# Performance work log

Measured on AMD Instinct MI355X. Metric: run time of the kernel, lower is better.

The kernel has to match this reference:

```python
import jax, jax.numpy as jnp
import numpy as np

N_NODES = 50000
N_EDGES = 800000
D = 128
N_GRAPHS = 64
N_CLASSES = 10


def setup_inputs() -> dict:
    key = jax.random.key(0)
    ks = jax.random.split(key, 10)
    x = jax.random.normal(ks[0], (N_NODES, D), dtype=jnp.float32)
    edge_index = jax.random.randint(ks[1], (2, N_EDGES), 0, N_NODES, dtype=jnp.int64)
    batch = jnp.sort(jax.random.randint(ks[2], (N_NODES,), 0, N_GRAPHS, dtype=jnp.int64))
    s = 1.0 / np.sqrt(D)
    W1a = jax.random.uniform(ks[3], (D, D), jnp.float32, -s, s)
    W1b = jax.random.uniform(ks[4], (D, D), jnp.float32, -s, s)
    W2a = jax.random.uniform(ks[5], (D, D), jnp.float32, -s, s)
    W2b = jax.random.uniform(ks[6], (D, D), jnp.float32, -s, s)
    Wfc = jax.random.uniform(ks[7], (D, N_CLASSES), jnp.float32, -s, s)
    return {
        "x": x, "edge_index": edge_index, "batch": batch,
        "W1a": W1a, "b1a": jnp.zeros((D,), jnp.float32),
        "W1b": W1b, "b1b": jnp.zeros((D,), jnp.float32),
        "W2a": W2a, "b2a": jnp.zeros((D,), jnp.float32),
        "W2b": W2b, "b2b": jnp.zeros((D,), jnp.float32),
        "Wfc": Wfc, "bfc": jnp.zeros((N_CLASSES,), jnp.float32),
    }


def _gin_conv(x, src, dst, Wa, ba, Wb, bb):
    # sum aggregation of neighbor messages x[src] into dst (eps = 0)
    agg = jax.ops.segment_sum(x[src], dst, num_segments=N_NODES)
    h = x + agg  # (1 + eps) * x + sum_{j->i} x_j
    h = jax.nn.relu(h @ Wa + ba)
    h = jax.nn.relu(h @ Wb + bb)
    return h


def reference(x, edge_index, batch, W1a, b1a, W1b, b1b, W2a, b2a, W2b, b2b, Wfc, bfc):
    src, dst = edge_index[0], edge_index[1]
    h = _gin_conv(x, src, dst, W1a, b1a, W1b, b1b)
    h = _gin_conv(h, src, dst, W2a, b2a, W2b, b2b)
    # global mean pool over graphs
    sums = jax.ops.segment_sum(h, batch, num_segments=N_GRAPHS)
    counts = jax.ops.segment_sum(jnp.ones((h.shape[0], 1), h.dtype), batch, num_segments=N_GRAPHS)
    pooled = sums / jnp.maximum(counts, 1.0)
    logits = pooled @ Wfc + bfc
    return jax.nn.sigmoid(logits)
```

## Files before the change

### kernel.cpp

```cpp
#include <hip/hip_runtime.h>

#define NN 50000
#define NE 800000
#define DF 128
#define NG 64
#define NC 10
#define NBK 98
#define PART_CHUNK 4096
#define PART_GRID 196
#define ACAP 12288
#define FINE_CAP 12288
#define RT 136
#define CAST_GRID 6250

typedef short bf16x8 __attribute__((ext_vector_type(8)));
typedef float f32x4  __attribute__((ext_vector_type(4)));

__device__ __forceinline__ void atomAddF(float* p, float v) {
  __hip_atomic_fetch_add(p, v, __ATOMIC_RELAXED, __HIP_MEMORY_SCOPE_AGENT);
}
__device__ __forceinline__ float b2f(unsigned short u) {
  union { unsigned int i; float f; } v; v.i = (unsigned int)u << 16; return v.f;
}
__device__ __forceinline__ unsigned int f2b(float f) {
  unsigned int i = __float_as_uint(f);
  return (i + 0x7fffu + ((i >> 16) & 1u)) >> 16;
}

__global__ __launch_bounds__(256) void k_prep(const float* __restrict__ x,
                                              unsigned short* __restrict__ xb,
                                              const float* __restrict__ W0,
                                              const float* __restrict__ W1,
                                              const float* __restrict__ W2,
                                              const float* __restrict__ W3,
                                              unsigned short* __restrict__ Wt)
{
  const int b = blockIdx.x;
  if (b < CAST_GRID) {
    const int i = b * 256 + threadIdx.x;
    const float4 v = reinterpret_cast<const float4*>(x)[i];
    uint2 o;
    o.x = f2b(v.x) | (f2b(v.y) << 16);
    o.y = f2b(v.z) | (f2b(v.w) << 16);
    reinterpret_cast<uint2*>(xb)[i] = o;
  } else {
    const int o = (b - CAST_GRID) * 256 + threadIdx.x;
    const int mat = o >> 11;
    const float* W = (mat == 0) ? W0 : (mat == 1) ? W1 : (mat == 2) ? W2 : W3;
    const int rem = o & 2047;
    const int kb = rem >> 7;
    const int n  = rem & 127;
    unsigned int u[8];
#pragma unroll
    for (int j = 0; j < 8; ++j) u[j] = f2b(W[(size_t)(kb * 8 + j) * DF + n]);
    uint4 p;
    p.x = u[0] | (u[1] << 16);
    p.y = u[2] | (u[3] << 16);
    p.z = u[4] | (u[5] << 16);
    p.w = u[6] | (u[7] << 16);
    *reinterpret_cast<uint4*>(Wt + (size_t)mat * DF * DF + (size_t)rem * 8) = p;
  }
}

__global__ __launch_bounds__(256) void k_part(const int* __restrict__ src,
                                              const int* __restrict__ dst,
                                              int* __restrict__ cnt_b,
                                              unsigned int* __restrict__ arena)
{
  __shared__ unsigned int stage[PART_CHUNK];
  __shared__ int lhist[128], lcnt[128], lcur[128], gbase[128];
  const int tid = threadIdx.x;
  const int e0  = blockIdx.x * PART_CHUNK;
  const int nE  = min(PART_CHUNK, NE - e0);

  for (int i = tid; i < 128; i += 256) lhist[i] = 0;
  __syncthreads();

  unsigned int pk[16];
  int bk[16];
#pragma unroll
  for (int i = 0; i < 16; ++i) {
    const int e = e0 + i * 256 + tid;
    if (e < NE) {
      const int d = dst[e];
      const int s = src[e];
      const int b = d >> 9;
      bk[i] = b;
      pk[i] = ((unsigned int)b << 25) | ((unsigned int)(d & 511) << 16) | (unsigned int)s;
      atomicAdd(&lhist[b], 1);
    } else {
      bk[i] = -1;
    }
  }
  __syncthreads();
  for (int i = tid; i < 128; i += 256) lcnt[i] = lhist[i];
  __syncthreads();
  for (int off = 1; off < 128; off <<= 1) {
    int v = 0;
    if (tid < 128 && tid >= off) v = lhist[tid - off];
    __syncthreads();
    if (tid < 128) lhist[tid] += v;
    __syncthreads();
  }
  if (tid < 128) lcur[tid] = lhist[tid] - lcnt[tid];
  __syncthreads();
#pragma unroll
  for (int i = 0; i < 16; ++i) {
    if (bk[i] >= 0) {
      const int pos = atomicAdd(&lcur[bk[i]], 1);
      stage[pos] = pk[i];
    }
  }
  __syncthreads();
  if (tid < NBK) {
    const int c = lcnt[tid];
    if (c > 0) gbase[tid] = atomicAdd(&cnt_b[tid], c);
  }
  __syncthreads();
  for (int idx = tid; idx < nE; idx += 256) {
    const unsigned int p = stage[idx];
    const int b = (int)(p >> 25);
    const int loff = lhist[b] - lcnt[b];
    arena[(size_t)b * ACAP + gbase[b] + (idx - loff)] = p;
  }
}

__global__ __launch_bounds__(128) void k_bscan(const int* __restrict__ cnt_b,
                                               int* __restrict__ base_b,
                                               int* __restrict__ rs)
{
  __shared__ int sm[128];
  const int t = threadIdx.x;
  const int v = (t < NBK) ? cnt_b[t] : 0;
  sm[t] = v;
  __syncthreads();
  for (int off = 1; off < 128; off <<= 1) {
    int u = (t >= off) ? sm[t - off] : 0;
    __syncthreads();
    sm[t] += u;
    __syncthreads();
  }
  base_b[t] = sm[t] - v;
  if (t == NBK - 1) rs[NN] = sm[t];
}

__global__ __launch_bounds__(256) void k_fine(const unsigned int* __restrict__ arena,
                                              const int* __restrict__ cnt_b,
                                              const int* __restrict__ base_b,
                                              int* __restrict__ rs,
                                              unsigned short* __restrict__ es)
{
  __shared__ unsigned short les[FINE_CAP];
  __shared__ int bins[4096];
  __shared__ int partials[256];
  const int tid   = threadIdx.x;
  const int b     = blockIdx.x;
  const int cnt   = cnt_b[b];
  const int wbase = base_b[b];
  const int nbase = b << 9;
  const int nwin  = min(512, NN - nbase);
  const unsigned int* ap = arena + (size_t)b * ACAP;

  for (int i = tid; i < 4096; i += 256) bins[i] = 0;
  __syncthreads();
  for (int idx = tid; idx < cnt; idx += 256) {
    const unsigned int p = ap[idx];
    const int key = (int)(((p >> 16) & 511) << 3) | (int)((p & 0xffffu) >> 13);
    atomicAdd(&bins[key], 1);
  }
  __syncthreads();
  const int b16 = tid * 16;
  int sum = 0;
#pragma unroll
  for (int k = 0; k < 16; ++k) sum += bins[b16 + k];
  partials[tid] = sum;
  __syncthreads();
  for (int off = 1; off < 256; off <<= 1) {
    int u = (tid >= off) ? partials[tid - off] : 0;
    __syncthreads();
    partials[tid] += u;
    __syncthreads();
  }
  int run = partials[tid] - sum;
#pragma unroll
  for (int k = 0; k < 16; ++k) {
    const int v = bins[b16 + k];
    bins[b16 + k] = run;
    run += v;
  }
  __syncthreads();
  for (int i = tid; i < nwin; i += 256) rs[nbase + i] = wbase + bins[i << 3];
  __syncthreads();
  if (cnt <= FINE_CAP) {
    for (int idx = tid; idx < cnt; idx += 256) {
      const unsigned int p = ap[idx];
      const int key = (int)(((p >> 16) & 511) << 3) | (int)((p & 0xffffu) >> 13);
      const int pos = atomicAdd(&bins[key], 1);
      les[pos] = (unsigned short)(p & 0xffffu);
    }
    __syncthreads();
    for (int i = tid; i < cnt; i += 256) es[wbase + i] = les[i];
  } else {
    for (int idx = tid; idx < cnt; idx += 256) {
      const unsigned int p = ap[idx];
      const int key = (int)(((p >> 16) & 511) << 3) | (int)((p & 0xffffu) >> 13);
      const int pos = atomicAdd(&bins[key], 1);
      es[wbase + pos] = (unsigned short)(p & 0xffffu);
    }
  }
}

__global__ __launch_bounds__(256) void k_gather(const unsigned short* __restrict__ feat,
                                                unsigned short* __restrict__ outp,
                                                const int* __restrict__ rs,
                                                const unsigned short* __restrict__ es)
{
  const int wid  = (blockIdx.x * 256 + threadIdx.x) >> 6;
  const int lane = threadIdx.x & 63;
  if (wid >= NN) return;
  const int beg = rs[wid];
  const int end = rs[wid + 1];
  const int off = lane * 2;

  const unsigned int self = *reinterpret_cast<const unsigned int*>(feat + (size_t)wid * DF + off);
  float ax = b2f(self & 0xffff), ay = b2f(self >> 16);
  int j = beg;
  while (j < end && (j & 3)) {
    const int s = es[j];
    const unsigned int u = *reinterpret_cast<const unsigned int*>(feat + (size_t)s * DF + off);
    ax += b2f(u & 0xffff);
    ay += b2f(u >> 16);
    ++j;
  }
  for (; j + 3 < end; j += 4) {
    const uint2 e4 = *reinterpret_cast<const uint2*>(es + j);
    const int s0 = (int)(e4.x & 0xffffu), s1 = (int)(e4.x >> 16);
    const int s2 = (int)(e4.y & 0xffffu), s3 = (int)(e4.y >> 16);
    const unsigned int u0 = *reinterpret_cast<const unsigned int*>(feat + (size_t)s0 * DF + off);
    const unsigned int u1 = *reinterpret_cast<const unsigned int*>(feat + (size_t)s1 * DF + off);
    const unsigned int u2 = *reinterpret_cast<const unsigned int*>(feat + (size_t)s2 * DF + off);
    const unsigned int u3 = *reinterpret_cast<const unsigned int*>(feat + (size_t)s3 * DF + off);
    ax += b2f(u0 & 0xffff) + b2f(u1 & 0xffff) + b2f(u2 & 0xffff) + b2f(u3 & 0xffff);
    ay += b2f(u0 >> 16)    + b2f(u1 >> 16)    + b2f(u2 >> 16)    + b2f(u3 >> 16);
  }
  for (; j < end; ++j) {
    const int s = es[j];
    const unsigned int u = *reinterpret_cast<const unsigned int*>(feat + (size_t)s * DF + off);
    ax += b2f(u & 0xffff);
    ay += b2f(u >> 16);
  }
  const unsigned int o = f2b(ax) | (f2b(ay) << 16);
  *reinterpret_cast<unsigned int*>(outp + (size_t)wid * DF + off) = o;
}

__global__ __launch_bounds__(256, 3) void k_gemm2(const unsigned short* __restrict__ Ab,
                                                  const unsigned short* __restrict__ Wta,
                                                  const float* __restrict__ ba,
                                                  const unsigned short* __restrict__ Wtb,
                                                  const float* __restrict__ bb,
                                                  unsigned short* __restrict__ outb, int M)
{
  __shared__ unsigned short WaL[2048 * 8];
  __shared__ unsigned short hL[4][16 * RT];
  const int tid  = threadIdx.x;
  const int lane = tid & 63;
  const int w    = tid >> 6;
  const int col  = lane & 15;
  const int kq   = lane >> 4;

#pragma unroll
  for (int i = 0; i < 8; ++i)
    *reinterpret_cast<uint4*>(&WaL[(i * 256 + tid) * 8]) =
        *reinterpret_cast<const uint4*>(&Wta[(size_t)(i * 256 + tid) * 8]);

  float4 bva[8], bvb[8];
#pragma unroll
  for (int nf = 0; nf < 8; ++nf) {
    bva[nf] = *reinterpret_cast<const float4*>(ba + nf * 16 + kq * 4);
    bvb[nf] = *reinterpret_cast<const float4*>(bb + nf * 16 + kq * 4);
  }

  const int m   = blockIdx.x * 64 + w * 16 + col;
  const int mld = (m < M) ? m : (M - 1);

  bf16x8 bc[4];
#pragma unroll
  for (int s = 0; s < 4; ++s)
    bc[s] = *reinterpret_cast<const bf16x8*>(Ab + (size_t)mld * DF + s * 32 + kq * 8);

  __syncthreads();

  f32x4 acc[8];
#pragma unroll
  for (int nf = 0; nf < 8; ++nf) acc[nf] = (f32x4){0.f, 0.f, 0.f, 0.f};
#pragma unroll
  for (int s = 0; s < 4; ++s) {
#pragma unroll
    for (int nf = 0; nf < 8; ++nf) {
      const bf16x8 wa = *reinterpret_cast<const bf16x8*>(
          &WaL[((s * 4 + kq) * 128 + nf * 16 + col) * 8]);
      acc[nf] = __builtin_amdgcn_mfma_f32_16x16x32_bf16(wa, bc[s], acc[nf], 0, 0, 0);
    }
  }

  unsigned short* hw = &hL[w][0];
#pragma unroll
  for (int nf = 0; nf < 8; ++nf) {
    uint2 pk;
    pk.x = f2b(fmaxf(acc[nf][0] + bva[nf].x, 0.f)) | (f2b(fmaxf(acc[nf][1] + bva[nf].y, 0.f)) << 16);
    pk.y = f2b(fmaxf(acc[nf][2] + bva[nf].z, 0.f)) | (f2b(fmaxf(acc[nf][3] + bva[nf].w, 0.f)) << 16);
    *reinterpret_cast<uint2*>(&hw[col * RT + nf * 16 + kq * 4]) = pk;
  }
  asm volatile("s_waitcnt lgkmcnt(0)" ::: "memory");
  __builtin_amdgcn_sched_barrier(0);

  f32x4 acc2[8];
#pragma unroll
  for (int nf = 0; nf < 8; ++nf) acc2[nf] = (f32x4){0.f, 0.f, 0.f, 0.f};
#pragma unroll
  for (int s = 0; s < 4; ++s) {
    const bf16x8 hb = *reinterpret_cast<const bf16x8*>(&hw[col * RT + s * 32 + kq * 8]);
#pragma unroll
    for (int nf = 0; nf < 8; ++nf) {
      const bf16x8 wb = *reinterpret_cast<const bf16x8*>(
          Wtb + ((size_t)(s * 4 + kq) * 128 + nf * 16 + col) * 8);
      acc2[nf] = __builtin_amdgcn_mfma_f32_16x16x32_bf16(wb, hb, acc2[nf], 0, 0, 0);
    }
  }
  if (m < M) {
#pragma unroll
    for (int nf = 0; nf < 8; ++nf) {
      ushort4 p;
      p.x = (unsigned short)f2b(fmaxf(acc2[nf][0] + bvb[nf].x, 0.f));
      p.y = (unsigned short)f2b(fmaxf(acc2[nf][1] + bvb[nf].y, 0.f));
      p.z = (unsigned short)f2b(fmaxf(acc2[nf][2] + bvb[nf].z, 0.f));
      p.w = (unsigned short)f2b(fmaxf(acc2[nf][3] + bvb[nf].w, 0.f));
      *reinterpret_cast<ushort4*>(outb + (size_t)m * DF + nf * 16 + kq * 4) = p;
    }
  }
}

__global__ __launch_bounds__(256) void k_pool(const unsigned short* __restrict__ h,
                                              const int* __restrict__ batch,
                                              float* __restrict__ sums,
                                              int* __restrict__ cnts)
{
  const int wv   = (blockIdx.x * 256 + threadIdx.x) >> 6;
  const int lane = threadIdx.x & 63;
  const int n0 = wv * 32;
  if (n0 >= NN) return;
  const int n1 = min(n0 + 32, NN);
  const int off = lane * 2;

  const int gfirst = batch[n0];
  const int glast  = batch[n1 - 1];
  float ax = 0.f, ay = 0.f;

  if (gfirst == glast) {
#pragma unroll 4
    for (int i = n0; i < n1; ++i) {
      const unsigned int u = *reinterpret_cast<const unsigned int*>(h + (size_t)i * DF + off);
      ax += b2f(u & 0xffff);
      ay += b2f(u >> 16);
    }
    atomAddF(&sums[gfirst * DF + off],     ax);
    atomAddF(&sums[gfirst * DF + off + 1], ay);
    if (lane == 0) atomicAdd(&cnts[gfirst], n1 - n0);
  } else {
    int g = gfirst, cnt = 0;
    for (int i = n0; i < n1; ++i) {
      const int gi = batch[i];
      if (gi != g) {
        atomAddF(&sums[g * DF + off],     ax);
        atomAddF(&sums[g * DF + off + 1], ay);
        if (lane == 0) atomicAdd(&cnts[g], cnt);
        ax = 0.f; ay = 0.f; cnt = 0; g = gi;
      }
      const unsigned int u = *reinterpret_cast<const unsigned int*>(h + (size_t)i * DF + off);
      ax += b2f(u & 0xffff);
      ay += b2f(u >> 16);
      ++cnt;
    }
    atomAddF(&sums[g * DF + off],     ax);
    atomAddF(&sums[g * DF + off + 1], ay);
    if (lane == 0) atomicAdd(&cnts[g], cnt);
  }
}

__global__ __launch_bounds__(256) void k_head(const float* __restrict__ sums,
                                              const int* __restrict__ cnts,
                                              const float* __restrict__ Wfc,
                                              const float* __restrict__ bfc,
                                              float* __restrict__ out)
{
  for (int o = threadIdx.x; o < NG * NC; o += 256) {
    const int g = o / NC, c = o % NC;
    const float inv = 1.f / fmaxf((float)cnts[g], 1.f);
    float z = bfc[c];
    for (int k = 0; k < DF; ++k)
      z = fmaf(sums[g * DF + k] * inv, Wfc[k * NC + c], z);
    out[o] = 1.f / (1.f + expf(-z));
  }
}

extern "C" void kernel_launch(void* const* d_in, const int* in_sizes, int n_in,
                              void* d_out, int out_size, void* d_ws, size_t ws_size,
                              hipStream_t stream)
{
  const float* x   = (const float*)d_in[0];
  const int*   ei  = (const int*)d_in[1];
  const int* batch = (const int*)d_in[2];
  const float* W1a = (const float*)d_in[3];
  const float* b1a = (const float*)d_in[4];
  const float* W1b = (const float*)d_in[5];
  const float* b1b = (const float*)d_in[6];
  const float* W2a = (const float*)d_in[7];
  const float* b2a = (const float*)d_in[8];
  const float* W2b = (const float*)d_in[9];
  const float* b2b = (const float*)d_in[10];
  const float* Wfc = (const float*)d_in[11];
  const float* bfc = (const float*)d_in[12];
  float* out = (float*)d_out;

  const int* src = ei;
  const int* dst = ei + NE;

  unsigned short* xb = (unsigned short*)d_ws;
  unsigned short* A  = xb + (size_t)NN * DF;
  unsigned short* H  = A + (size_t)NN * DF;
  unsigned short* Wt = H + (size_t)NN * DF;
  float* sums  = (float*)(Wt + (size_t)4 * DF * DF);
  int*   cnts  = (int*)(sums + NG * DF);
  int*   cnt_b = cnts + 64;
  int*   base_b= cnt_b + 128;
  int*   rs    = base_b + 128;
  unsigned short* es = (unsigned short*)(rs + (NN + 4));
  unsigned int* arena = (unsigned int*)(es + NE);

  unsigned short* Wt1a = Wt;
  unsigned short* Wt1b = Wt + DF * DF;
  unsigned short* Wt2a = Wt + 2 * DF * DF;
  unsigned short* Wt2b = Wt + 3 * DF * DF;

  const int gemm_grid   = (NN + 63) / 64;
  const int gather_grid = (NN * 64 + 255) / 256;
  const int pool_grid   = ((NN + 31) / 32 + 3) / 4;

  k_prep<<<CAST_GRID + 32, 256, 0, stream>>>(x, xb, W1a, W1b, W2a, W2b, Wt);
  hipMemsetAsync(sums, 0, (size_t)(NG * DF + 64 + 128) * sizeof(float), stream);
  k_part<<<PART_GRID, 256, 0, stream>>>(src, dst, cnt_b, arena);
  k_bscan<<<1, 128, 0, stream>>>(cnt_b, base_b, rs);
  k_fine<<<NBK, 256, 0, stream>>>(arena, cnt_b, base_b, rs, es);

  k_gather<<<gather_grid, 256, 0, stream>>>(xb, A, rs, es);
  k_gemm2<<<gemm_grid, 256, 0, stream>>>(A, Wt1a, b1a, Wt1b, b1b, A, NN);

  k_gather<<<gather_grid, 256, 0, stream>>>(A, H, rs, es);
  k_gemm2<<<gemm_grid, 256, 0, stream>>>(H, Wt2a, b2a, Wt2b, b2b, H, NN);

  k_pool<<<pool_grid, 256, 0, stream>>>(H, batch, sums, cnts);
  k_head<<<1, 256, 0, stream>>>(sums, cnts, Wfc, bfc, out);
}
```

Before: 192.9 us.

## Fuse prep and partition kernels, fold bucket scan into fine sort, drop GEMM LDS staging

Merges the bf16 cast/weight-transpose kernel and the edge-partition kernel into one launch, selected by block index. The bucket prefix-scan kernel is removed: each fine-sort block recomputes the 98-entry scan in shared memory, and rs[NN] is set to NE directly. In the two-layer GEMM, the first weight matrix is read straight from global memory instead of being staged in LDS, and bias values are loaded where they are used; this frees shared memory and registers so the launch bound allows 4 blocks per CU. This removes two launch gaps and the per-block LDS weight fill, but the cast blocks of the fused kernel now reserve the partition kernel's shared memory, and the weight operands come through the cache instead of LDS.

New measurement: 196.0 us. About the same (+1.6%).

```diff
diff --git a/kernel.cpp b/kernel.cpp
--- a/kernel.cpp
+++ b/kernel.cpp
@@ -12,6 +12,7 @@
 #define FINE_CAP 12288
 #define RT 136
 #define CAST_GRID 6250
+#define PREP_GRID (CAST_GRID + 32)
 
 typedef short bf16x8 __attribute__((ext_vector_type(8)));
 typedef float f32x4  __attribute__((ext_vector_type(4)));
@@ -27,29 +28,38 @@
   return (i + 0x7fffu + ((i >> 16) & 1u)) >> 16;
 }
 
-__global__ __launch_bounds__(256) void k_prep(const float* __restrict__ x,
-                                              unsigned short* __restrict__ xb,
-                                              const float* __restrict__ W0,
-                                              const float* __restrict__ W1,
-                                              const float* __restrict__ W2,
-                                              const float* __restrict__ W3,
-                                              unsigned short* __restrict__ Wt)
-{
-  const int b = blockIdx.x;
+__global__ __launch_bounds__(256) void k_prep_part(const float* __restrict__ x,
+                                                   unsigned short* __restrict__ xb,
+                                                   const float* __restrict__ W0,
+                                                   const float* __restrict__ W1,
+                                                   const float* __restrict__ W2,
+                                                   const float* __restrict__ W3,
+                                                   unsigned short* __restrict__ Wt,
+                                                   const int* __restrict__ src,
+                                                   const int* __restrict__ dst,
+                                                   int* __restrict__ cnt_b,
+                                                   unsigned int* __restrict__ arena)
+{
+  __shared__ unsigned int stage[PART_CHUNK];
+  __shared__ int lhist[128], lcnt[128], lcur[128], gbase[128];
+  const int tid = threadIdx.x;
+  const int b   = blockIdx.x;
+
   if (b < CAST_GRID) {
-    const int i = b * 256 + threadIdx.x;
+    const int i = b * 256 + tid;
     const float4 v = reinterpret_cast<const float4*>(x)[i];
     uint2 o;
     o.x = f2b(v.x) | (f2b(v.y) << 16);
     o.y = f2b(v.z) | (f2b(v.w) << 16);
     reinterpret_cast<uint2*>(xb)[i] = o;
-  } else {
-    const int o = (b - CAST_GRID) * 256 + threadIdx.x;
+    return;
+  }
+  if (b < PREP_GRID) {
+    const int o = (b - CAST_GRID) * 256 + tid;
     const int mat = o >> 11;
     const float* W = (mat == 0) ? W0 : (mat == 1) ? W1 : (mat == 2) ? W2 : W3;
     const int rem = o & 2047;
-    const int kb = rem >> 7;
-    const int n  = rem & 127;
+    const int kb = rem >> 7, n = rem & 127;
     unsigned int u[8];
 #pragma unroll
     for (int j = 0; j < 8; ++j) u[j] = f2b(W[(size_t)(kb * 8 + j) * DF + n]);
@@ -59,38 +69,26 @@
     p.z = u[4] | (u[5] << 16);
     p.w = u[6] | (u[7] << 16);
     *reinterpret_cast<uint4*>(Wt + (size_t)mat * DF * DF + (size_t)rem * 8) = p;
-  }
-}
-
-__global__ __launch_bounds__(256) void k_part(const int* __restrict__ src,
-                                              const int* __restrict__ dst,
-                                              int* __restrict__ cnt_b,
-                                              unsigned int* __restrict__ arena)
-{
-  __shared__ unsigned int stage[PART_CHUNK];
-  __shared__ int lhist[128], lcnt[128], lcur[128], gbase[128];
-  const int tid = threadIdx.x;
-  const int e0  = blockIdx.x * PART_CHUNK;
-  const int nE  = min(PART_CHUNK, NE - e0);
+    return;
+  }
+
+  const int vb = b - PREP_GRID;
+  const int e0 = vb * PART_CHUNK;
+  const int nE = min(PART_CHUNK, NE - e0);
 
   for (int i = tid; i < 128; i += 256) lhist[i] = 0;
   __syncthreads();
-
-  unsigned int pk[16];
-  int bk[16];
+  unsigned int pk[16]; int bk[16];
 #pragma unroll
   for (int i = 0; i < 16; ++i) {
     const int e = e0 + i * 256 + tid;
     if (e < NE) {
-      const int d = dst[e];
-      const int s = src[e];
-      const int b = d >> 9;
-      bk[i] = b;
-      pk[i] = ((unsigned int)b << 25) | ((unsigned int)(d & 511) << 16) | (unsigned int)s;
-      atomicAdd(&lhist[b], 1);
-    } else {
-      bk[i] = -1;
-    }
+      const int d = dst[e], s = src[e];
+      const int bb = d >> 9;
+      bk[i] = bb;
+      pk[i] = ((unsigned int)bb << 25) | ((unsigned int)(d & 511) << 16) | (unsigned int)s;
+      atomicAdd(&lhist[bb], 1);
+    } else bk[i] = -1;
   }
   __syncthreads();
   for (int i = tid; i < 128; i += 256) lcnt[i] = lhist[i];
@@ -105,12 +103,11 @@
   if (tid < 128) lcur[tid] = lhist[tid] - lcnt[tid];
   __syncthreads();
 #pragma unroll
-  for (int i = 0; i < 16; ++i) {
+  for (int i = 0; i < 16; ++i)
     if (bk[i] >= 0) {
       const int pos = atomicAdd(&lcur[bk[i]], 1);
       stage[pos] = pk[i];
     }
-  }
   __syncthreads();
   if (tid < NBK) {
     const int c = lcnt[tid];
@@ -119,44 +116,37 @@
   __syncthreads();
   for (int idx = tid; idx < nE; idx += 256) {
     const unsigned int p = stage[idx];
-    const int b = (int)(p >> 25);
-    const int loff = lhist[b] - lcnt[b];
-    arena[(size_t)b * ACAP + gbase[b] + (idx - loff)] = p;
-  }
-}
-
-__global__ __launch_bounds__(128) void k_bscan(const int* __restrict__ cnt_b,
-                                               int* __restrict__ base_b,
-                                               int* __restrict__ rs)
-{
-  __shared__ int sm[128];
-  const int t = threadIdx.x;
-  const int v = (t < NBK) ? cnt_b[t] : 0;
-  sm[t] = v;
-  __syncthreads();
-  for (int off = 1; off < 128; off <<= 1) {
-    int u = (t >= off) ? sm[t - off] : 0;
-    __syncthreads();
-    sm[t] += u;
-    __syncthreads();
-  }
-  base_b[t] = sm[t] - v;
-  if (t == NBK - 1) rs[NN] = sm[t];
+    const int bb = (int)(p >> 25);
+    const int loff = lhist[bb] - lcnt[bb];
+    arena[(size_t)bb * ACAP + gbase[bb] + (idx - loff)] = p;
+  }
 }
 
 __global__ __launch_bounds__(256) void k_fine(const unsigned int* __restrict__ arena,
                                               const int* __restrict__ cnt_b,
-                                              const int* __restrict__ base_b,
                                               int* __restrict__ rs,
                                               unsigned short* __restrict__ es)
 {
   __shared__ unsigned short les[FINE_CAP];
   __shared__ int bins[4096];
   __shared__ int partials[256];
-  const int tid   = threadIdx.x;
-  const int b     = blockIdx.x;
+  __shared__ int basebuf[128];
+  const int tid = threadIdx.x;
+  const int b   = blockIdx.x;
+
+  if (b == 0 && tid == 0) rs[NN] = NE;
+
+  if (tid < 128) basebuf[tid] = (tid < NBK) ? cnt_b[tid] : 0;
+  __syncthreads();
+  for (int off = 1; off < 128; off <<= 1) {
+    int u = 0;
+    if (tid < 128 && tid >= off) u = basebuf[tid - off];
+    __syncthreads();
+    if (tid < 128) basebuf[tid] += u;
+    __syncthreads();
+  }
+  const int wbase = (b == 0) ? 0 : basebuf[b - 1];
   const int cnt   = cnt_b[b];
-  const int wbase = base_b[b];
   const int nbase = b << 9;
   const int nwin  = min(512, NN - nbase);
   const unsigned int* ap = arena + (size_t)b * ACAP;
@@ -226,10 +216,8 @@
   float ax = b2f(self & 0xffff), ay = b2f(self >> 16);
   int j = beg;
   while (j < end && (j & 3)) {
-    const int s = es[j];
-    const unsigned int u = *reinterpret_cast<const unsigned int*>(feat + (size_t)s * DF + off);
-    ax += b2f(u & 0xffff);
-    ay += b2f(u >> 16);
+    const unsigned int u = *reinterpret_cast<const unsigned int*>(feat + (size_t)es[j] * DF + off);
+    ax += b2f(u & 0xffff); ay += b2f(u >> 16);
     ++j;
   }
   for (; j + 3 < end; j += 4) {
@@ -244,23 +232,20 @@
     ay += b2f(u0 >> 16)    + b2f(u1 >> 16)    + b2f(u2 >> 16)    + b2f(u3 >> 16);
   }
   for (; j < end; ++j) {
-    const int s = es[j];
-    const unsigned int u = *reinterpret_cast<const unsigned int*>(feat + (size_t)s * DF + off);
-    ax += b2f(u & 0xffff);
-    ay += b2f(u >> 16);
+    const unsigned int u = *reinterpret_cast<const unsigned int*>(feat + (size_t)es[j] * DF + off);
+    ax += b2f(u & 0xffff); ay += b2f(u >> 16);
   }
   const unsigned int o = f2b(ax) | (f2b(ay) << 16);
   *reinterpret_cast<unsigned int*>(outp + (size_t)wid * DF + off) = o;
 }
 
-__global__ __launch_bounds__(256, 3) void k_gemm2(const unsigned short* __restrict__ Ab,
+__global__ __launch_bounds__(256, 4) void k_gemm2(const unsigned short* __restrict__ Ab,
                                                   const unsigned short* __restrict__ Wta,
                                                   const float* __restrict__ ba,
                                                   const unsigned short* __restrict__ Wtb,
                                                   const float* __restrict__ bb,
                                                   unsigned short* __restrict__ outb, int M)
 {
-  __shared__ unsigned short WaL[2048 * 8];
   __shared__ unsigned short hL[4][16 * RT];
   const int tid  = threadIdx.x;
   const int lane = tid & 63;
@@ -268,18 +253,6 @@
   const int col  = lane & 15;
   const int kq   = lane >> 4;
 
-#pragma unroll
-  for (int i = 0; i < 8; ++i)
-    *reinterpret_cast<uint4*>(&WaL[(i * 256 + tid) * 8]) =
-        *reinterpret_cast<const uint4*>(&Wta[(size_t)(i * 256 + tid) * 8]);
-
-  float4 bva[8], bvb[8];
-#pragma unroll
-  for (int nf = 0; nf < 8; ++nf) {
-    bva[nf] = *reinterpret_cast<const float4*>(ba + nf * 16 + kq * 4);
-    bvb[nf] = *reinterpret_cast<const float4*>(bb + nf * 16 + kq * 4);
-  }
-
   const int m   = blockIdx.x * 64 + w * 16 + col;
   const int mld = (m < M) ? m : (M - 1);
 
@@ -288,8 +261,6 @@
   for (int s = 0; s < 4; ++s)
     bc[s] = *reinterpret_cast<const bf16x8*>(Ab + (size_t)mld * DF + s * 32 + kq * 8);
 
-  __syncthreads();
-
   f32x4 acc[8];
 #pragma unroll
   for (int nf = 0; nf < 8; ++nf) acc[nf] = (f32x4){0.f, 0.f, 0.f, 0.f};
@@ -298,7 +269,7 @@
 #pragma unroll
     for (int nf = 0; nf < 8; ++nf) {
       const bf16x8 wa = *reinterpret_cast<const bf16x8*>(
-          &WaL[((s * 4 + kq) * 128 + nf * 16 + col) * 8]);
+          Wta + ((size_t)(s * 4 + kq) * 128 + nf * 16 + col) * 8);
       acc[nf] = __builtin_amdgcn_mfma_f32_16x16x32_bf16(wa, bc[s], acc[nf], 0, 0, 0);
     }
   }
@@ -306,9 +277,10 @@
   unsigned short* hw = &hL[w][0];
 #pragma unroll
   for (int nf = 0; nf < 8; ++nf) {
+    const float4 bva = *reinterpret_cast<const float4*>(ba + nf * 16 + kq * 4);
     uint2 pk;
-    pk.x = f2b(fmaxf(acc[nf][0] + bva[nf].x, 0.f)) | (f2b(fmaxf(acc[nf][1] + bva[nf].y, 0.f)) << 16);
-    pk.y = f2b(fmaxf(acc[nf][2] + bva[nf].z, 0.f)) | (f2b(fmaxf(acc[nf][3] + bva[nf].w, 0.f)) << 16);
+    pk.x = f2b(fmaxf(acc[nf][0] + bva.x, 0.f)) | (f2b(fmaxf(acc[nf][1] + bva.y, 0.f)) << 16);
+    pk.y = f2b(fmaxf(acc[nf][2] + bva.z, 0.f)) | (f2b(fmaxf(acc[nf][3] + bva.w, 0.f)) << 16);
     *reinterpret_cast<uint2*>(&hw[col * RT + nf * 16 + kq * 4]) = pk;
   }
   asm volatile("s_waitcnt lgkmcnt(0)" ::: "memory");
@@ -330,11 +302,12 @@
   if (m < M) {
 #pragma unroll
     for (int nf = 0; nf < 8; ++nf) {
+      const float4 bvb = *reinterpret_cast<const float4*>(bb + nf * 16 + kq * 4);
       ushort4 p;
-      p.x = (unsigned short)f2b(fmaxf(acc2[nf][0] + bvb[nf].x, 0.f));
-      p.y = (unsigned short)f2b(fmaxf(acc2[nf][1] + bvb[nf].y, 0.f));
-      p.z = (unsigned short)f2b(fmaxf(acc2[nf][2] + bvb[nf].z, 0.f));
-      p.w = (unsigned short)f2b(fmaxf(acc2[nf][3] + bvb[nf].w, 0.f));
+      p.x = (unsigned short)f2b(fmaxf(acc2[nf][0] + bvb.x, 0.f));
+      p.y = (unsigned short)f2b(fmaxf(acc2[nf][1] + bvb.y, 0.f));
+      p.z = (unsigned short)f2b(fmaxf(acc2[nf][2] + bvb.z, 0.f));
+      p.w = (unsigned short)f2b(fmaxf(acc2[nf][3] + bvb.w, 0.f));
       *reinterpret_cast<ushort4*>(outb + (size_t)m * DF + nf * 16 + kq * 4) = p;
     }
   }
@@ -360,8 +333,7 @@
 #pragma unroll 4
     for (int i = n0; i < n1; ++i) {
       const unsigned int u = *reinterpret_cast<const unsigned int*>(h + (size_t)i * DF + off);
-      ax += b2f(u & 0xffff);
-      ay += b2f(u >> 16);
+      ax += b2f(u & 0xffff); ay += b2f(u >> 16);
     }
     atomAddF(&sums[gfirst * DF + off],     ax);
     atomAddF(&sums[gfirst * DF + off + 1], ay);
@@ -377,8 +349,7 @@
         ax = 0.f; ay = 0.f; cnt = 0; g = gi;
       }
       const unsigned int u = *reinterpret_cast<const unsigned int*>(h + (size_t)i * DF + off);
-      ax += b2f(u & 0xffff);
-      ay += b2f(u >> 16);
+      ax += b2f(u & 0xffff); ay += b2f(u >> 16);
       ++cnt;
     }
     atomAddF(&sums[g * DF + off],     ax);
@@ -432,8 +403,7 @@
   float* sums  = (float*)(Wt + (size_t)4 * DF * DF);
   int*   cnts  = (int*)(sums + NG * DF);
   int*   cnt_b = cnts + 64;
-  int*   base_b= cnt_b + 128;
-  int*   rs    = base_b + 128;
+  int*   rs    = cnt_b + 128;
   unsigned short* es = (unsigned short*)(rs + (NN + 4));
   unsigned int* arena = (unsigned int*)(es + NE);
 
@@ -446,11 +416,10 @@
   const int gather_grid = (NN * 64 + 255) / 256;
   const int pool_grid   = ((NN + 31) / 32 + 3) / 4;
 
-  k_prep<<<CAST_GRID + 32, 256, 0, stream>>>(x, xb, W1a, W1b, W2a, W2b, Wt);
   hipMemsetAsync(sums, 0, (size_t)(NG * DF + 64 + 128) * sizeof(float), stream);
-  k_part<<<PART_GRID, 256, 0, stream>>>(src, dst, cnt_b, arena);
-  k_bscan<<<1, 128, 0, stream>>>(cnt_b, base_b, rs);
-  k_fine<<<NBK, 256, 0, stream>>>(arena, cnt_b, base_b, rs, es);
+  k_prep_part<<<PREP_GRID + PART_GRID, 256, 0, stream>>>(
+      x, xb, W1a, W1b, W2a, W2b, Wt, src, dst, cnt_b, arena);
+  k_fine<<<NBK, 256, 0, stream>>>(arena, cnt_b, rs, es);
 
   k_gather<<<gather_grid, 256, 0, stream>>>(xb, A, rs, es);
   k_gemm2<<<gemm_grid, 256, 0, stream>>>(A, Wt1a, b1a, Wt1b, b1b, A, NN);
```
